# Optimization experiments

Measured on AMD Instinct MI355X. Metric: run time of the kernel, lower is better.

The kernel has to match this reference:

```python
import jax, jax.numpy as jnp
import numpy as np

B, C, H, P = 8, 3, 384, 16
DIM, DEPTH, HEADS, MLP = 768, 8, 12, 3072
NP_ = (H // P) ** 2  # 576 patches
PD = C * P * P       # patch_dim = 768
EPS = 1e-5


def _ln(x, g, b):
    m = jnp.mean(x, axis=-1, keepdims=True)
    v = jnp.mean((x - m) ** 2, axis=-1, keepdims=True)
    return (x - m) / jnp.sqrt(v + EPS) * g + b


def setup_inputs() -> dict:
    key = jax.random.key(0)
    ks = jax.random.split(key, 16)
    s = 0.02
    return {
        "img": jax.random.normal(ks[0], (B, C, H, H), jnp.float32),
        "pos_embedding": jax.random.normal(ks[1], (1, NP_ + 1, DIM), jnp.float32),
        "cls_token": jax.random.normal(ks[2], (1, 1, DIM), jnp.float32),
        "patch_w": jax.random.normal(ks[3], (PD, DIM), jnp.float32) * s,
        "patch_b": jnp.zeros((DIM,), jnp.float32),
        "ln1_g": jnp.ones((DEPTH, DIM), jnp.float32),
        "ln1_b": jnp.zeros((DEPTH, DIM), jnp.float32),
        "qkv_w": jax.random.normal(ks[4], (DEPTH, DIM, 3 * DIM), jnp.float32) * s,
        "out_w": jax.random.normal(ks[5], (DEPTH, DIM, DIM), jnp.float32) * s,
        "out_b": jnp.zeros((DEPTH, DIM), jnp.float32),
        "ln2_g": jnp.ones((DEPTH, DIM), jnp.float32),
        "ln2_b": jnp.zeros((DEPTH, DIM), jnp.float32),
        "ff1_w": jax.random.normal(ks[6], (DEPTH, DIM, MLP), jnp.float32) * s,
        "ff1_b": jnp.zeros((DEPTH, MLP), jnp.float32),
        "ff2_w": jax.random.normal(ks[7], (DEPTH, MLP, DIM), jnp.float32) * s,
        "ff2_b": jnp.zeros((DEPTH, DIM), jnp.float32),
    }


def reference(img, pos_embedding, cls_token, patch_w, patch_b,
              ln1_g, ln1_b, qkv_w, out_w, out_b,
              ln2_g, ln2_b, ff1_w, ff1_b, ff2_w, ff2_b):
    b = img.shape[0]
    hp = H // P
    # b c (h p1) (w p2) -> b (h w) (p1 p2 c)
    x = img.reshape(b, C, hp, P, hp, P).transpose(0, 2, 4, 3, 5, 1).reshape(b, hp * hp, P * P * C)
    x = x @ patch_w + patch_b
    x = jnp.concatenate([jnp.broadcast_to(cls_token, (b, 1, DIM)), x], axis=1)
    x = x + pos_embedding[:, : x.shape[1]]

    def layer(xc, p):
        g1, b1, wqkv, wo, bo, g2, b2, w1, bf1, w2, bf2 = p
        y = _ln(xc, g1, b1)
        qkv = y @ wqkv
        q, k, v = jnp.split(qkv, 3, axis=-1)
        sp = lambda a: a.reshape(b, -1, HEADS, DIM // HEADS).transpose(0, 2, 1, 3)
        q, k, v = sp(q), sp(k), sp(v)
        # NOTE: original code never applies the 1/sqrt(d) scale -- faithful.
        dots = jnp.einsum('bhid,bhjd->bhij', q, k)
        attn = jax.nn.softmax(dots, axis=-1)
        o = jnp.einsum('bhij,bhjd->bhid', attn, v).transpose(0, 2, 1, 3).reshape(b, -1, DIM)
        xc = xc + (o @ wo + bo)
        y = _ln(xc, g2, b2)
        xc = xc + (jax.nn.gelu(y @ w1 + bf1, approximate=False) @ w2 + bf2)
        return xc, None

    x, _ = jax.lax.scan(layer, x, (ln1_g, ln1_b, qkv_w, out_w, out_b,
                                   ln2_g, ln2_b, ff1_w, ff1_b, ff2_w, ff2_b))
    return x[:, 1:, :]
```

## Files before the change

kernel.cpp:

```cpp
#include <hip/hip_runtime.h>
#include <hip/hip_bf16.h>
#include <math.h>

#define BB 8
#define CC 3
#define HH 384
#define PP 16
#define HP 24
#define NP 576
#define PD 768
#define DIM 768
#define DEPTH 8
#define HEADS 12
#define DH 64
#define MLP 3072
#define SS 577
#define BS (BB*SS)
#define MPAD 4736
#define LN_EPS 1e-5f
#define NKT 10
#define QW (3*DIM)

typedef __attribute__((ext_vector_type(8))) short s8v;
typedef __attribute__((ext_vector_type(4))) float f4v;

__device__ __forceinline__ float bf2f(unsigned short s) {
    union { unsigned u; float f; } x;
    x.u = ((unsigned)s) << 16;
    return x.f;
}
__device__ __forceinline__ unsigned short f2bfu(float f) {
    __hip_bfloat16 h = __float2bfloat16(f);
    return *reinterpret_cast<unsigned short*>(&h);
}

__device__ __forceinline__ void async16(void* lds, const void* g) {
    __builtin_amdgcn_global_load_lds(
        (const __attribute__((address_space(1))) void*)(uintptr_t)g,
        (__attribute__((address_space(3))) void*)(unsigned)(uintptr_t)lds,
        16, 0, 0);
}

__global__ __launch_bounds__(256) void patchify_k(const float* __restrict__ img,
                                                  unsigned short* __restrict__ xp) {
    int idx = blockIdx.x * 256 + threadIdx.x;
    const int total = BB * NP * PD;
    if (idx >= total) return;
    int b = idx / (NP * PD);
    int r = idx % (NP * PD);
    int n = r / PD;
    int j = r % PD;
    int c  = j % CC;
    int t  = j / CC;
    int p2 = t % PP;
    int p1 = t / PP;
    int hh = n / HP;
    int ww = n % HP;
    int row = hh * PP + p1;
    int col = ww * PP + p2;
    xp[idx] = f2bfu(img[(((size_t)b * CC + c) * HH + row) * HH + col]);
}

__global__ __launch_bounds__(256) void convT_k(const float* __restrict__ W,
                                               unsigned short* __restrict__ Wt,
                                               int K, int N) {
    __shared__ float t[32][33];
    int tx = threadIdx.x & 31, ty = threadIdx.x >> 5;
    int n0 = blockIdx.x * 32, k0 = blockIdx.y * 32;
#pragma unroll
    for (int i = 0; i < 32; i += 8)
        t[ty + i][tx] = W[(size_t)(k0 + ty + i) * N + n0 + tx];
    __syncthreads();
#pragma unroll
    for (int i = 0; i < 32; i += 8)
        Wt[(size_t)(n0 + ty + i) * K + k0 + tx] = f2bfu(t[tx][ty + i]);
}

__global__ __launch_bounds__(256) void convT4_k(const float* __restrict__ s0,
                                                const float* __restrict__ s1,
                                                const float* __restrict__ s2,
                                                const float* __restrict__ s3,
                                                unsigned short* __restrict__ d0,
                                                unsigned short* __restrict__ d1,
                                                unsigned short* __restrict__ d2,
                                                unsigned short* __restrict__ d3) {
    __shared__ float t[32][33];
    int bid = blockIdx.x;
    const float* S; unsigned short* D; int K, N, lt;
    if (bid < 1728)      { S = s0; D = d0; K = 768;  N = 2304; lt = bid; }
    else if (bid < 2304) { S = s1; D = d1; K = 768;  N = 768;  lt = bid - 1728; }
    else if (bid < 4608) { S = s2; D = d2; K = 768;  N = 3072; lt = bid - 2304; }
    else                 { S = s3; D = d3; K = 3072; N = 768;  lt = bid - 4608; }
    int ntn = N >> 5;
    int n0 = (lt % ntn) * 32, k0 = (lt / ntn) * 32;
    int tx = threadIdx.x & 31, ty = threadIdx.x >> 5;
#pragma unroll
    for (int i = 0; i < 32; i += 8)
        t[ty + i][tx] = S[(size_t)(k0 + ty + i) * N + n0 + tx];
    __syncthreads();
#pragma unroll
    for (int i = 0; i < 32; i += 8)
        D[(size_t)(n0 + ty + i) * K + k0 + tx] = f2bfu(t[tx][ty + i]);
}

__global__ __launch_bounds__(256) void build_x_k(const float* __restrict__ pe,
                                                 const float* __restrict__ cls,
                                                 const float* __restrict__ pos,
                                                 float* __restrict__ x) {
    int idx = blockIdx.x * 256 + threadIdx.x;
    const int total = BB * SS * DIM;
    if (idx >= total) return;
    int b = idx / (SS * DIM);
    int r = idx % (SS * DIM);
    int i = r / DIM;
    int d = r % DIM;
    float p = pos[i * DIM + d];
    float v = (i == 0) ? cls[d] : pe[((size_t)b * NP + (i - 1)) * DIM + d];
    x[idx] = v + p;
}

template <int NPART>
__global__ __launch_bounds__(256) void ln_k(const float* __restrict__ x,
                                            const float* __restrict__ P,
                                            const float* __restrict__ g,
                                            const float* __restrict__ bt,
                                            unsigned short* __restrict__ y,
                                            float* __restrict__ xout) {
    __shared__ float sm[8];
    int row = blockIdx.x, tid = threadIdx.x;
    const float* xr = x + (size_t)row * DIM;
    float v0 = xr[tid], v1 = xr[tid + 256], v2 = xr[tid + 512];
    if (NPART == 2) {
        const float* p0 = P + (size_t)row * DIM;
        const float* p1 = P + (size_t)(BS + row) * DIM;
        v0 += p0[tid]       + p1[tid];
        v1 += p0[tid + 256] + p1[tid + 256];
        v2 += p0[tid + 512] + p1[tid + 512];
        float* xo = xout + (size_t)row * DIM;
        xo[tid] = v0; xo[tid + 256] = v1; xo[tid + 512] = v2;
    }
    float s = v0 + v1 + v2;
    for (int o = 32; o; o >>= 1) s += __shfl_xor(s, o);
    if ((tid & 63) == 0) sm[tid >> 6] = s;
    __syncthreads();
    float mean = (sm[0] + sm[1] + sm[2] + sm[3]) * (1.f / 768.f);
    float q0 = v0 - mean, q1 = v1 - mean, q2 = v2 - mean;
    float s2 = q0 * q0 + q1 * q1 + q2 * q2;
    for (int o = 32; o; o >>= 1) s2 += __shfl_xor(s2, o);
    if ((tid & 63) == 0) sm[4 + (tid >> 6)] = s2;
    __syncthreads();
    float var = (sm[4] + sm[5] + sm[6] + sm[7]) * (1.f / 768.f);
    float rstd = rsqrtf(var + LN_EPS);
    unsigned short* yr = y + (size_t)row * DIM;
    yr[tid]       = f2bfu(q0 * rstd * g[tid]       + bt[tid]);
    yr[tid + 256] = f2bfu(q1 * rstd * g[tid + 256] + bt[tid + 256]);
    yr[tid + 512] = f2bfu(q2 * rstd * g[tid + 512] + bt[tid + 512]);
}

template <int OP, int SPLIT>
__global__ __launch_bounds__(256) void mgemm_k(const unsigned short* __restrict__ A,
                                               const unsigned short* __restrict__ Bt,
                                               const float* __restrict__ bias,
                                               void* __restrict__ Cv,
                                               int M, int N, int K) {
    __shared__ unsigned short Al[3][128 * 32];
    __shared__ unsigned short Bl[3][128 * 32];
    int tid = threadIdx.x;
    int wv = tid >> 6, lane = tid & 63;
    int quad = lane >> 4, l16 = lane & 15;
    int m0 = blockIdx.y * 128, n0 = blockIdx.x * 128;
    int wm = (wv >> 1) * 64, wn = (wv & 1) * 64;
    int rg = lane >> 2;
    int kc = (((lane & 3) ^ (rg & 3)) * 8);
    int rslot = ((quad ^ (l16 & 3)) * 8);

    const int Ks = K / SPLIT;
    const int kbase = blockIdx.z * Ks;
    const int T = Ks / 32;

    f4v acc[4][4];
    const f4v zero = {0.f, 0.f, 0.f, 0.f};
#pragma unroll
    for (int i = 0; i < 4; ++i)
#pragma unroll
        for (int j = 0; j < 4; ++j) acc[i][j] = zero;

    auto stage = [&](int t, int bufi) {
#pragma unroll
        for (int gg = 0; gg < 2; ++gg) {
            int g = wv + gg * 4;
            const unsigned short* ga =
                A + (size_t)(m0 + g * 16 + rg) * K + kbase + t * 32 + kc;
            async16(&Al[bufi][g * 512], ga);
            const unsigned short* gb =
                Bt + (size_t)(n0 + g * 16 + rg) * K + kbase + t * 32 + kc;
            async16(&Bl[bufi][g * 512], gb);
        }
    };

    auto compute = [&](int cur) {
        s8v af[4], bfr[4];
#pragma unroll
        for (int i = 0; i < 4; ++i)
            af[i] = *reinterpret_cast<const s8v*>(&Al[cur][(wm + i * 16 + l16) * 32 + rslot]);
#pragma unroll
        for (int j = 0; j < 4; ++j)
            bfr[j] = *reinterpret_cast<const s8v*>(&Bl[cur][(wn + j * 16 + l16) * 32 + rslot]);
        __builtin_amdgcn_s_setprio(1);
#pragma unroll
        for (int i = 0; i < 4; ++i)
#pragma unroll
            for (int j = 0; j < 4; ++j)
                acc[i][j] = __builtin_amdgcn_mfma_f32_16x16x32_bf16(af[i], bfr[j], acc[i][j], 0, 0, 0);
        __builtin_amdgcn_s_setprio(0);
    };

    stage(0, 0);
    stage(1, 1);

    int cur = 0, pre = 2;
    for (int t = 0; t < T - 1; ++t) {
        asm volatile("s_waitcnt vmcnt(4)" ::: "memory");
        __builtin_amdgcn_s_barrier();
        asm volatile("" ::: "memory");
        if (t + 2 < T) stage(t + 2, pre);
        compute(cur);
        cur = (cur == 2) ? 0 : cur + 1;
        pre = (pre == 2) ? 0 : pre + 1;
    }
    asm volatile("s_waitcnt vmcnt(0)" ::: "memory");
    __builtin_amdgcn_s_barrier();
    asm volatile("" ::: "memory");
    compute(cur);

#pragma unroll
    for (int j = 0; j < 4; ++j) {
        int col = n0 + wn + j * 16 + l16;
        float bj = bias ? bias[col] : 0.f;
        if (SPLIT > 1 && blockIdx.z != 0) bj = 0.f;
#pragma unroll
        for (int i = 0; i < 4; ++i) {
#pragma unroll
            for (int r = 0; r < 4; ++r) {
                int row = m0 + wm + i * 16 + quad * 4 + r;
                if (row >= M) continue;
                float v = acc[i][j][r] + bj;
                size_t idx = (size_t)row * N + col;
                if (OP == 0) {
                    ((unsigned short*)Cv)[idx] = f2bfu(v);
                } else if (OP == 1) {
                    v = 0.5f * v * (1.f + erff(v * 0.70710678118654752f));
                    ((unsigned short*)Cv)[idx] = f2bfu(v);
                } else if (OP == 2) {
                    float* C = (float*)Cv;
                    if (SPLIT > 1) atomicAdd(&C[idx], v);
                    else C[idx] += v;
                } else if (OP == 3) {
                    ((float*)Cv)[idx] = v;
                } else {
                    float* C = (float*)Cv + (size_t)blockIdx.z * ((size_t)M * N);
                    C[idx] = v;
                }
            }
        }
    }
}

__global__ __launch_bounds__(256) void mattn_k(const unsigned short* __restrict__ qkv,
                                               unsigned short* __restrict__ o) {
    __shared__ unsigned short Kl[64 * 72];
    __shared__ unsigned short Vt[64 * 72];
    __shared__ unsigned short Pw[4][16 * 72];

    int tid = threadIdx.x;
    int w = tid >> 6, lane = tid & 63, quad = lane >> 4, l16 = lane & 15;
    int bh = blockIdx.x;
    int b = bh / HEADS, h = bh % HEADS;
    int q0 = blockIdx.y * 64;

    int qq = q0 + w * 16 + l16;
    if (qq > SS - 1) qq = SS - 1;
    const unsigned short* qp = qkv + (size_t)(b * SS + qq) * QW + h * DH + quad * 8;
    s8v aq0 = *reinterpret_cast<const s8v*>(qp);
    s8v aq1 = *reinterpret_cast<const s8v*>(qp + 32);

    float m[4], l[4];
    f4v O[4];
    const f4v zero = {0.f, 0.f, 0.f, 0.f};
#pragma unroll
    for (int r = 0; r < 4; ++r) { m[r] = -INFINITY; l[r] = 0.f; }
#pragma unroll
    for (int dg = 0; dg < 4; ++dg) O[dg] = zero;

    for (int t = 0; t < NKT; ++t) {
        int k0 = t * 64;
        __syncthreads();
#pragma unroll
        for (int rr = 0; rr < 2; ++rr) {
            int cid = tid + rr * 256;
            int row = cid >> 3, cb = (cid & 7) * 8;
            s8v kv = *reinterpret_cast<const s8v*>(
                qkv + (size_t)(b * SS + k0 + row) * QW + DIM + h * DH + cb);
            *reinterpret_cast<s8v*>(&Kl[row * 72 + cb]) = kv;
        }
        {
            int kb = (tid & 15) * 4, db = (tid >> 4) * 4;
            const unsigned short* vb = qkv + (size_t)(b * SS + k0 + kb) * QW + 2 * DIM + h * DH + db;
            ushort4 r0 = *reinterpret_cast<const ushort4*>(vb);
            ushort4 r1 = *reinterpret_cast<const ushort4*>(vb + QW);
            ushort4 r2 = *reinterpret_cast<const ushort4*>(vb + 2 * QW);
            ushort4 r3 = *reinterpret_cast<const ushort4*>(vb + 3 * QW);
            ushort4 w0 = {r0.x, r1.x, r2.x, r3.x};
            ushort4 w1 = {r0.y, r1.y, r2.y, r3.y};
            ushort4 w2 = {r0.z, r1.z, r2.z, r3.z};
            ushort4 w3 = {r0.w, r1.w, r2.w, r3.w};
            *reinterpret_cast<ushort4*>(&Vt[(db + 0) * 72 + kb]) = w0;
            *reinterpret_cast<ushort4*>(&Vt[(db + 1) * 72 + kb]) = w1;
            *reinterpret_cast<ushort4*>(&Vt[(db + 2) * 72 + kb]) = w2;
            *reinterpret_cast<ushort4*>(&Vt[(db + 3) * 72 + kb]) = w3;
        }
        __syncthreads();

        f4v s[4];
#pragma unroll
        for (int kk = 0; kk < 4; ++kk) {
            const unsigned short* kp = &Kl[(kk * 16 + l16) * 72 + quad * 8];
            s8v b0 = *reinterpret_cast<const s8v*>(kp);
            s8v b1 = *reinterpret_cast<const s8v*>(kp + 32);
            f4v z = zero;
            z = __builtin_amdgcn_mfma_f32_16x16x32_bf16(aq0, b0, z, 0, 0, 0);
            z = __builtin_amdgcn_mfma_f32_16x16x32_bf16(aq1, b1, z, 0, 0, 0);
            s[kk] = z;
        }
        int kvalid = SS - k0;
        if (kvalid < 64) {
#pragma unroll
            for (int kk = 0; kk < 4; ++kk)
                if (kk * 16 + l16 >= kvalid) {
                    f4v mk = {-1e30f, -1e30f, -1e30f, -1e30f};
                    s[kk] = mk;
                }
        }
        float alpha[4];
#pragma unroll
        for (int r = 0; r < 4; ++r) {
            float mx = fmaxf(fmaxf(s[0][r], s[1][r]), fmaxf(s[2][r], s[3][r]));
#pragma unroll
            for (int off = 1; off < 16; off <<= 1) mx = fmaxf(mx, __shfl_xor(mx, off));
            float mn = fmaxf(m[r], mx);
            alpha[r] = __expf(m[r] - mn);
            m[r] = mn;
            float ps = 0.f;
#pragma unroll
            for (int kk = 0; kk < 4; ++kk) {
                float p = __expf(s[kk][r] - mn);
                ps += p;
                Pw[w][(quad * 4 + r) * 72 + kk * 16 + l16] = f2bfu(p);
            }
#pragma unroll
            for (int off = 1; off < 16; off <<= 1) ps += __shfl_xor(ps, off);
            l[r] = l[r] * alpha[r] + ps;
        }
#pragma unroll
        for (int dg = 0; dg < 4; ++dg)
#pragma unroll
            for (int r = 0; r < 4; ++r) O[dg][r] *= alpha[r];

        s8v ap0 = *reinterpret_cast<const s8v*>(&Pw[w][l16 * 72 + quad * 8]);
        s8v ap1 = *reinterpret_cast<const s8v*>(&Pw[w][l16 * 72 + 32 + quad * 8]);
#pragma unroll
        for (int dg = 0; dg < 4; ++dg) {
            const unsigned short* vp = &Vt[(dg * 16 + l16) * 72 + quad * 8];
            s8v bv0 = *reinterpret_cast<const s8v*>(vp);
            s8v bv1 = *reinterpret_cast<const s8v*>(vp + 32);
            O[dg] = __builtin_amdgcn_mfma_f32_16x16x32_bf16(ap0, bv0, O[dg], 0, 0, 0);
            O[dg] = __builtin_amdgcn_mfma_f32_16x16x32_bf16(ap1, bv1, O[dg], 0, 0, 0);
        }
    }

#pragma unroll
    for (int r = 0; r < 4; ++r) {
        int q = q0 + w * 16 + quad * 4 + r;
        if (q >= SS) continue;
        float inv = 1.f / l[r];
        unsigned short* op = o + (size_t)(b * SS + q) * DIM + h * DH + l16;
#pragma unroll
        for (int dg = 0; dg < 4; ++dg)
            op[dg * 16] = f2bfu(O[dg][r] * inv);
    }
}

template <int NPART>
__global__ __launch_bounds__(256) void copy_out_k(const float* __restrict__ x,
                                                  const float* __restrict__ P,
                                                  float* __restrict__ out) {
    int idx = blockIdx.x * 256 + threadIdx.x;
    const int total = BB * NP * DIM;
    if (idx >= total) return;
    int b = idx / (NP * DIM);
    int r = idx % (NP * DIM);
    int n = r / DIM;
    int d = r % DIM;
    size_t row = (size_t)b * SS + 1 + n;
    float v = x[row * DIM + d];
    if (NPART == 2)
        v += P[row * DIM + d] + P[(size_t)BS * DIM + row * DIM + d];
    out[idx] = v;
}

extern "C" void kernel_launch(void* const* d_in, const int* in_sizes, int n_in,
                              void* d_out, int out_size, void* d_ws, size_t ws_size,
                              hipStream_t stream) {
    const float* img     = (const float*)d_in[0];
    const float* pos     = (const float*)d_in[1];
    const float* cls     = (const float*)d_in[2];
    const float* patch_w = (const float*)d_in[3];
    const float* patch_b = (const float*)d_in[4];
    const float* ln1_g   = (const float*)d_in[5];
    const float* ln1_b   = (const float*)d_in[6];
    const float* qkv_w   = (const float*)d_in[7];
    const float* out_w   = (const float*)d_in[8];
    const float* out_b   = (const float*)d_in[9];
    const float* ln2_g   = (const float*)d_in[10];
    const float* ln2_b   = (const float*)d_in[11];
    const float* ff1_w   = (const float*)d_in[12];
    const float* ff1_b   = (const float*)d_in[13];
    const float* ff2_w   = (const float*)d_in[14];
    const float* ff2_b   = (const float*)d_in[15];
    float* out = (float*)d_out;

    char* base = (char*)d_ws;
    float* x = (float*)base;                          base += (size_t)BS * DIM * 4;
    unsigned short* y_bf   = (unsigned short*)base;   base += (size_t)MPAD * DIM * 2;
    unsigned short* t1_bf  = (unsigned short*)base;   base += (size_t)MPAD * DIM * 2;
    unsigned short* qkv_bf = (unsigned short*)base;   base += (size_t)MPAD * 3 * DIM * 2;
    unsigned short* hid_bf = (unsigned short*)base;   base += (size_t)MPAD * MLP * 2;
    unsigned short* xp_bf  = (unsigned short*)base;   base += (size_t)BB * NP * PD * 2;
    unsigned short* wq_t = (unsigned short*)base;     base += (size_t)(3 * DIM) * DIM * 2;
    unsigned short* wo_t = (unsigned short*)base;     base += (size_t)DIM * DIM * 2;
    unsigned short* w1_t = (unsigned short*)base;     base += (size_t)MLP * DIM * 2;
    unsigned short* w2_t = (unsigned short*)base;     base += (size_t)DIM * MLP * 2;
    float* part = (float*)base;                       base += (size_t)2 * BS * DIM * 4;
    float* pe_f32 = (float*)hid_bf;

    const int threads = 256;
    const int mblk = (BS + 127) / 128;

    patchify_k<<<(BB * NP * PD + 255) / 256, threads, 0, stream>>>(img, xp_bf);
    convT_k<<<dim3(DIM / 32, PD / 32), threads, 0, stream>>>(patch_w, wq_t, PD, DIM);
    mgemm_k<3, 1><<<dim3(DIM / 128, (BB * NP) / 128), threads, 0, stream>>>(
        xp_bf, wq_t, patch_b, pe_f32, BB * NP, DIM, PD);
    build_x_k<<<(BB * SS * DIM + 255) / 256, threads, 0, stream>>>(pe_f32, cls, pos, x);

    for (int l = 0; l < DEPTH; ++l) {
        if (l == 0)
            ln_k<0><<<BS, threads, 0, stream>>>(x, nullptr, ln1_g, ln1_b, y_bf, nullptr);
        else
            ln_k<2><<<BS, threads, 0, stream>>>(x, part, ln1_g + l * DIM, ln1_b + l * DIM,
                                                y_bf, x);
        convT4_k<<<6912, threads, 0, stream>>>(
            qkv_w + (size_t)l * DIM * 3 * DIM,
            out_w + (size_t)l * DIM * DIM,
            ff1_w + (size_t)l * DIM * MLP,
            ff2_w + (size_t)l * MLP * DIM,
            wq_t, wo_t, w1_t, w2_t);
        mgemm_k<0, 1><<<dim3(3 * DIM / 128, mblk), threads, 0, stream>>>(
            y_bf, wq_t, nullptr, qkv_bf, BS, 3 * DIM, DIM);
        mattn_k<<<dim3(BB * HEADS, NKT), threads, 0, stream>>>(qkv_bf, t1_bf);
        mgemm_k<4, 2><<<dim3(DIM / 128, mblk, 2), threads, 0, stream>>>(
            t1_bf, wo_t, out_b + l * DIM, part, BS, DIM, DIM);
        ln_k<2><<<BS, threads, 0, stream>>>(x, part, ln2_g + l * DIM, ln2_b + l * DIM,
                                            y_bf, x);
        mgemm_k<1, 1><<<dim3(MLP / 128, mblk), threads, 0, stream>>>(
            y_bf, w1_t, ff1_b + l * MLP, hid_bf, BS, MLP, DIM);
        mgemm_k<4, 2><<<dim3(DIM / 128, mblk, 2), threads, 0, stream>>>(
            hid_bf, w2_t, ff2_b + l * DIM, part, BS, DIM, MLP);
    }

    copy_out_k<2><<<(BB * NP * DIM + 255) / 256, threads, 0, stream>>>(x, part, out);
}
```

Baseline: 1.997 ms.

## Remap GEMM blocks across XCDs, simplify LDS layout, split FF2 GEMM four ways

The GEMM now remaps linear block IDs so that consecutive tiles are spread round-robin across the 8 XCDs, aiming for better L2 locality. It also drops the XOR-swizzled LDS layout in favour of a contiguous per-lane 16-row-group layout. The FF2 GEMM moves from split-K 2 to split-K 4. The two extra partial buffers reuse the t1/qkv workspace, and the next LayerNorm and the final copy sum four partials instead of two. This adds more fp32 partial traffic and relies on the aliased workspace being dead at that point. The unswizzled LDS layout may bring back bank conflicts.

```diff
diff --git a/kernel.cpp b/kernel.cpp
--- a/kernel.cpp
+++ b/kernel.cpp
@@ -122,6 +122,7 @@
 template <int NPART>
 __global__ __launch_bounds__(256) void ln_k(const float* __restrict__ x,
                                             const float* __restrict__ P,
+                                            const float* __restrict__ P2,
                                             const float* __restrict__ g,
                                             const float* __restrict__ bt,
                                             unsigned short* __restrict__ y,
@@ -130,12 +131,19 @@
     int row = blockIdx.x, tid = threadIdx.x;
     const float* xr = x + (size_t)row * DIM;
     float v0 = xr[tid], v1 = xr[tid + 256], v2 = xr[tid + 512];
-    if (NPART == 2) {
+    if (NPART >= 2) {
         const float* p0 = P + (size_t)row * DIM;
         const float* p1 = P + (size_t)(BS + row) * DIM;
         v0 += p0[tid]       + p1[tid];
         v1 += p0[tid + 256] + p1[tid + 256];
         v2 += p0[tid + 512] + p1[tid + 512];
+        if (NPART == 4) {
+            const float* p2 = P2 + (size_t)row * DIM;
+            const float* p3 = P2 + (size_t)(BS + row) * DIM;
+            v0 += p2[tid]       + p3[tid];
+            v1 += p2[tid + 256] + p3[tid + 256];
+            v2 += p2[tid + 512] + p3[tid + 512];
+        }
         float* xo = xout + (size_t)row * DIM;
         xo[tid] = v0; xo[tid + 256] = v1; xo[tid + 512] = v2;
     }
@@ -162,17 +170,23 @@
                                                const unsigned short* __restrict__ Bt,
                                                const float* __restrict__ bias,
                                                void* __restrict__ Cv,
+                                               void* __restrict__ Cv2,
                                                int M, int N, int K) {
     __shared__ unsigned short Al[3][128 * 32];
     __shared__ unsigned short Bl[3][128 * 32];
     int tid = threadIdx.x;
     int wv = tid >> 6, lane = tid & 63;
     int quad = lane >> 4, l16 = lane & 15;
-    int m0 = blockIdx.y * 128, n0 = blockIdx.x * 128;
+
+    int nb = gridDim.x * gridDim.y;
+    int p  = blockIdx.x + gridDim.x * blockIdx.y;
+    int u = p & 7, i8 = p >> 3;
+    int q8 = nb >> 3, r8 = nb & 7;
+    int w = (u < r8 ? u * (q8 + 1) : r8 * (q8 + 1) + (u - r8) * q8) + i8;
+    int bx = w % gridDim.x, by = w / gridDim.x;
+
+    int m0 = by * 128, n0 = bx * 128;
     int wm = (wv >> 1) * 64, wn = (wv & 1) * 64;
-    int rg = lane >> 2;
-    int kc = (((lane & 3) ^ (rg & 3)) * 8);
-    int rslot = ((quad ^ (l16 & 3)) * 8);
 
     const int Ks = K / SPLIT;
     const int kbase = blockIdx.z * Ks;
@@ -190,22 +204,23 @@
         for (int gg = 0; gg < 2; ++gg) {
             int g = wv + gg * 4;
             const unsigned short* ga =
-                A + (size_t)(m0 + g * 16 + rg) * K + kbase + t * 32 + kc;
+                A + (size_t)(m0 + g * 16 + l16) * K + kbase + t * 32 + quad * 8;
             async16(&Al[bufi][g * 512], ga);
             const unsigned short* gb =
-                Bt + (size_t)(n0 + g * 16 + rg) * K + kbase + t * 32 + kc;
+                Bt + (size_t)(n0 + g * 16 + l16) * K + kbase + t * 32 + quad * 8;
             async16(&Bl[bufi][g * 512], gb);
         }
     };
 
     auto compute = [&](int cur) {
         s8v af[4], bfr[4];
+        int lo = lane * 8;
 #pragma unroll
         for (int i = 0; i < 4; ++i)
-            af[i] = *reinterpret_cast<const s8v*>(&Al[cur][(wm + i * 16 + l16) * 32 + rslot]);
+            af[i] = *reinterpret_cast<const s8v*>(&Al[cur][((wm >> 4) + i) * 512 + lo]);
 #pragma unroll
         for (int j = 0; j < 4; ++j)
-            bfr[j] = *reinterpret_cast<const s8v*>(&Bl[cur][(wn + j * 16 + l16) * 32 + rslot]);
+            bfr[j] = *reinterpret_cast<const s8v*>(&Bl[cur][((wn >> 4) + j) * 512 + lo]);
         __builtin_amdgcn_s_setprio(1);
 #pragma unroll
         for (int i = 0; i < 4; ++i)
@@ -258,7 +273,8 @@
                 } else if (OP == 3) {
                     ((float*)Cv)[idx] = v;
                 } else {
-                    float* C = (float*)Cv + (size_t)blockIdx.z * ((size_t)M * N);
+                    float* base = (float*)((SPLIT > 2 && blockIdx.z >= 2) ? Cv2 : Cv);
+                    float* C = base + (size_t)(blockIdx.z & 1) * ((size_t)M * N);
                     C[idx] = v;
                 }
             }
@@ -393,6 +409,7 @@
 template <int NPART>
 __global__ __launch_bounds__(256) void copy_out_k(const float* __restrict__ x,
                                                   const float* __restrict__ P,
+                                                  const float* __restrict__ P2,
                                                   float* __restrict__ out) {
     int idx = blockIdx.x * 256 + threadIdx.x;
     const int total = BB * NP * DIM;
@@ -403,8 +420,10 @@
     int d = r % DIM;
     size_t row = (size_t)b * SS + 1 + n;
     float v = x[row * DIM + d];
-    if (NPART == 2)
+    if (NPART >= 2)
         v += P[row * DIM + d] + P[(size_t)BS * DIM + row * DIM + d];
+    if (NPART == 4)
+        v += P2[row * DIM + d] + P2[(size_t)BS * DIM + row * DIM + d];
     out[idx] = v;
 }
 
@@ -441,6 +460,7 @@
     unsigned short* w1_t = (unsigned short*)base;     base += (size_t)MLP * DIM * 2;
     unsigned short* w2_t = (unsigned short*)base;     base += (size_t)DIM * MLP * 2;
     float* part = (float*)base;                       base += (size_t)2 * BS * DIM * 4;
+    float* part23 = (float*)t1_bf;
     float* pe_f32 = (float*)hid_bf;
 
     const int threads = 256;
@@ -449,14 +469,16 @@
     patchify_k<<<(BB * NP * PD + 255) / 256, threads, 0, stream>>>(img, xp_bf);
     convT_k<<<dim3(DIM / 32, PD / 32), threads, 0, stream>>>(patch_w, wq_t, PD, DIM);
     mgemm_k<3, 1><<<dim3(DIM / 128, (BB * NP) / 128), threads, 0, stream>>>(
-        xp_bf, wq_t, patch_b, pe_f32, BB * NP, DIM, PD);
+        xp_bf, wq_t, patch_b, pe_f32, nullptr, BB * NP, DIM, PD);
     build_x_k<<<(BB * SS * DIM + 255) / 256, threads, 0, stream>>>(pe_f32, cls, pos, x);
 
     for (int l = 0; l < DEPTH; ++l) {
         if (l == 0)
-            ln_k<0><<<BS, threads, 0, stream>>>(x, nullptr, ln1_g, ln1_b, y_bf, nullptr);
+            ln_k<0><<<BS, threads, 0, stream>>>(x, nullptr, nullptr, ln1_g, ln1_b,
+                                                y_bf, nullptr);
         else
-            ln_k<2><<<BS, threads, 0, stream>>>(x, part, ln1_g + l * DIM, ln1_b + l * DIM,
+            ln_k<4><<<BS, threads, 0, stream>>>(x, part, part23,
+                                                ln1_g + l * DIM, ln1_b + l * DIM,
                                                 y_bf, x);
         convT4_k<<<6912, threads, 0, stream>>>(
             qkv_w + (size_t)l * DIM * 3 * DIM,
@@ -465,17 +487,18 @@
             ff2_w + (size_t)l * MLP * DIM,
             wq_t, wo_t, w1_t, w2_t);
         mgemm_k<0, 1><<<dim3(3 * DIM / 128, mblk), threads, 0, stream>>>(
-            y_bf, wq_t, nullptr, qkv_bf, BS, 3 * DIM, DIM);
+            y_bf, wq_t, nullptr, qkv_bf, nullptr, BS, 3 * DIM, DIM);
         mattn_k<<<dim3(BB * HEADS, NKT), threads, 0, stream>>>(qkv_bf, t1_bf);
         mgemm_k<4, 2><<<dim3(DIM / 128, mblk, 2), threads, 0, stream>>>(
-            t1_bf, wo_t, out_b + l * DIM, part, BS, DIM, DIM);
-        ln_k<2><<<BS, threads, 0, stream>>>(x, part, ln2_g + l * DIM, ln2_b + l * DIM,
+            t1_bf, wo_t, out_b + l * DIM, part, nullptr, BS, DIM, DIM);
+        ln_k<2><<<BS, threads, 0, stream>>>(x, part, nullptr,
+                                            ln2_g + l * DIM, ln2_b + l * DIM,
                                             y_bf, x);
         mgemm_k<1, 1><<<dim3(MLP / 128, mblk), threads, 0, stream>>>(
-            y_bf, w1_t, ff1_b + l * MLP, hid_bf, BS, MLP, DIM);
-        mgemm_k<4, 2><<<dim3(DIM / 128, mblk, 2), threads, 0, stream>>>(
-            hid_bf, w2_t, ff2_b + l * DIM, part, BS, DIM, MLP);
+            y_bf, w1_t, ff1_b + l * MLP, hid_bf, nullptr, BS, MLP, DIM);
+        mgemm_k<4, 4><<<dim3(DIM / 128, mblk, 4), threads, 0, stream>>>(
+            hid_bf, w2_t, ff2_b + l * DIM, part, part23, BS, DIM, MLP);
     }
 
-    copy_out_k<2><<<(BB * NP * DIM + 255) / 256, threads, 0, stream>>>(x, part, out);
-}
+    copy_out_k<4><<<(BB * NP * DIM + 255) / 256, threads, 0, stream>>>(x, part, part23, out);
+}
```

Result: slower. 2.328 ms (+16.6%).

## Use 8-wave 512-thread GEMM blocks with 64x32 per-wave tiles

Applied to the files above, without the earlier changes.

The bf16 MFMA GEMM now launches 512 threads (8 waves) per 128x128 block, each wave computing a 64x32 sub-tile instead of 64x64. Each thread issues one async load per operand per k-step, and the vmcnt wait is adjusted to match. The XOR LDS swizzle is removed in favour of plain linear addressing. This is meant to add waves for latency hiding and cut per-wave accumulator registers, at the cost of more LDS fragment reads per MFMA and possible LDS bank conflicts.

```diff
diff --git a/kernel.cpp b/kernel.cpp
--- a/kernel.cpp
+++ b/kernel.cpp
@@ -158,7 +158,7 @@
 }
 
 template <int OP, int SPLIT>
-__global__ __launch_bounds__(256) void mgemm_k(const unsigned short* __restrict__ A,
+__global__ __launch_bounds__(512) void mgemm_k(const unsigned short* __restrict__ A,
                                                const unsigned short* __restrict__ Bt,
                                                const float* __restrict__ bias,
                                                void* __restrict__ Cv,
@@ -169,48 +169,43 @@
     int wv = tid >> 6, lane = tid & 63;
     int quad = lane >> 4, l16 = lane & 15;
     int m0 = blockIdx.y * 128, n0 = blockIdx.x * 128;
-    int wm = (wv >> 1) * 64, wn = (wv & 1) * 64;
+    int wm = (wv >> 2) * 64, wn = (wv & 3) * 32;
     int rg = lane >> 2;
-    int kc = (((lane & 3) ^ (rg & 3)) * 8);
-    int rslot = ((quad ^ (l16 & 3)) * 8);
+    int kc = (lane & 3) * 8;
 
     const int Ks = K / SPLIT;
     const int kbase = blockIdx.z * Ks;
     const int T = Ks / 32;
 
-    f4v acc[4][4];
+    f4v acc[4][2];
     const f4v zero = {0.f, 0.f, 0.f, 0.f};
 #pragma unroll
     for (int i = 0; i < 4; ++i)
 #pragma unroll
-        for (int j = 0; j < 4; ++j) acc[i][j] = zero;
+        for (int j = 0; j < 2; ++j) acc[i][j] = zero;
 
     auto stage = [&](int t, int bufi) {
-#pragma unroll
-        for (int gg = 0; gg < 2; ++gg) {
-            int g = wv + gg * 4;
-            const unsigned short* ga =
-                A + (size_t)(m0 + g * 16 + rg) * K + kbase + t * 32 + kc;
-            async16(&Al[bufi][g * 512], ga);
-            const unsigned short* gb =
-                Bt + (size_t)(n0 + g * 16 + rg) * K + kbase + t * 32 + kc;
-            async16(&Bl[bufi][g * 512], gb);
-        }
+        const unsigned short* ga =
+            A + (size_t)(m0 + wv * 16 + rg) * K + kbase + t * 32 + kc;
+        async16(&Al[bufi][wv * 512], ga);
+        const unsigned short* gb =
+            Bt + (size_t)(n0 + wv * 16 + rg) * K + kbase + t * 32 + kc;
+        async16(&Bl[bufi][wv * 512], gb);
     };
 
     auto compute = [&](int cur) {
-        s8v af[4], bfr[4];
+        s8v af[4], bfr[2];
 #pragma unroll
         for (int i = 0; i < 4; ++i)
-            af[i] = *reinterpret_cast<const s8v*>(&Al[cur][(wm + i * 16 + l16) * 32 + rslot]);
-#pragma unroll
-        for (int j = 0; j < 4; ++j)
-            bfr[j] = *reinterpret_cast<const s8v*>(&Bl[cur][(wn + j * 16 + l16) * 32 + rslot]);
+            af[i] = *reinterpret_cast<const s8v*>(&Al[cur][(wm + i * 16 + l16) * 32 + quad * 8]);
+#pragma unroll
+        for (int j = 0; j < 2; ++j)
+            bfr[j] = *reinterpret_cast<const s8v*>(&Bl[cur][(wn + j * 16 + l16) * 32 + quad * 8]);
         __builtin_amdgcn_s_setprio(1);
 #pragma unroll
         for (int i = 0; i < 4; ++i)
 #pragma unroll
-            for (int j = 0; j < 4; ++j)
+            for (int j = 0; j < 2; ++j)
                 acc[i][j] = __builtin_amdgcn_mfma_f32_16x16x32_bf16(af[i], bfr[j], acc[i][j], 0, 0, 0);
         __builtin_amdgcn_s_setprio(0);
     };
@@ -220,7 +215,7 @@
 
     int cur = 0, pre = 2;
     for (int t = 0; t < T - 1; ++t) {
-        asm volatile("s_waitcnt vmcnt(4)" ::: "memory");
+        asm volatile("s_waitcnt vmcnt(2)" ::: "memory");
         __builtin_amdgcn_s_barrier();
         asm volatile("" ::: "memory");
         if (t + 2 < T) stage(t + 2, pre);
@@ -234,7 +229,7 @@
     compute(cur);
 
 #pragma unroll
-    for (int j = 0; j < 4; ++j) {
+    for (int j = 0; j < 2; ++j) {
         int col = n0 + wn + j * 16 + l16;
         float bj = bias ? bias[col] : 0.f;
         if (SPLIT > 1 && blockIdx.z != 0) bj = 0.f;
@@ -444,11 +439,12 @@
     float* pe_f32 = (float*)hid_bf;
 
     const int threads = 256;
+    const int gthreads = 512;
     const int mblk = (BS + 127) / 128;
 
     patchify_k<<<(BB * NP * PD + 255) / 256, threads, 0, stream>>>(img, xp_bf);
     convT_k<<<dim3(DIM / 32, PD / 32), threads, 0, stream>>>(patch_w, wq_t, PD, DIM);
-    mgemm_k<3, 1><<<dim3(DIM / 128, (BB * NP) / 128), threads, 0, stream>>>(
+    mgemm_k<3, 1><<<dim3(DIM / 128, (BB * NP) / 128), gthreads, 0, stream>>>(
         xp_bf, wq_t, patch_b, pe_f32, BB * NP, DIM, PD);
     build_x_k<<<(BB * SS * DIM + 255) / 256, threads, 0, stream>>>(pe_f32, cls, pos, x);
 
@@ -464,16 +460,16 @@
             ff1_w + (size_t)l * DIM * MLP,
             ff2_w + (size_t)l * MLP * DIM,
             wq_t, wo_t, w1_t, w2_t);
-        mgemm_k<0, 1><<<dim3(3 * DIM / 128, mblk), threads, 0, stream>>>(
+        mgemm_k<0, 1><<<dim3(3 * DIM / 128, mblk), gthreads, 0, stream>>>(
             y_bf, wq_t, nullptr, qkv_bf, BS, 3 * DIM, DIM);
         mattn_k<<<dim3(BB * HEADS, NKT), threads, 0, stream>>>(qkv_bf, t1_bf);
-        mgemm_k<4, 2><<<dim3(DIM / 128, mblk, 2), threads, 0, stream>>>(
+        mgemm_k<4, 2><<<dim3(DIM / 128, mblk, 2), gthreads, 0, stream>>>(
             t1_bf, wo_t, out_b + l * DIM, part, BS, DIM, DIM);
         ln_k<2><<<BS, threads, 0, stream>>>(x, part, ln2_g + l * DIM, ln2_b + l * DIM,
                                             y_bf, x);
-        mgemm_k<1, 1><<<dim3(MLP / 128, mblk), threads, 0, stream>>>(
+        mgemm_k<1, 1><<<dim3(MLP / 128, mblk), gthreads, 0, stream>>>(
             y_bf, w1_t, ff1_b + l * MLP, hid_bf, BS, MLP, DIM);
-        mgemm_k<4, 2><<<dim3(DIM / 128, mblk, 2), threads, 0, stream>>>(
+        mgemm_k<4, 2><<<dim3(DIM / 128, mblk, 2), gthreads, 0, stream>>>(
             hid_bf, w2_t, ff2_b + l * DIM, part, BS, DIM, MLP);
     }
 
```

Measured after the change: 1.821 ms. 8.8% less time.
